# Optimization experiments

Hardware: AMD Instinct MI355X
Metric: run time of the kernel (lower is better)

## Reference

```python
import jax, jax.numpy as jnp
import numpy as np

N, E = 25000, 400000
D, H, L = 64, 4, 3
DH = D  # per-head out dim (concat=False averages heads)
NODE_IN, EDGE_IN = 16, 4


def setup_inputs() -> dict:
    key = jax.random.key(0)
    ks = jax.random.split(key, 24)
    s = 0.05
    inp = {
        "node_feat_in": jax.random.normal(ks[0], (N, NODE_IN), jnp.float32),
        "edge_index_in": jax.random.randint(ks[1], (2, E), 0, N, jnp.int32),
        "edge_attr_in": jax.random.normal(ks[2], (E, EDGE_IN), jnp.float32),
        # initial embeddings
        "W_node": jax.random.normal(ks[3], (NODE_IN, D), jnp.float32) * s,
        "b_node": jnp.zeros((D,), jnp.float32),
        "W_edge": jax.random.normal(ks[4], (EDGE_IN, D), jnp.float32) * s,
        "b_edge": jnp.zeros((D,), jnp.float32),
        # GATv2Conv params, stacked over layers
        "Wl": jax.random.normal(ks[5], (L, D, H * DH), jnp.float32) * s,
        "bl": jnp.zeros((L, H * DH), jnp.float32),
        "Wr": jax.random.normal(ks[6], (L, D, H * DH), jnp.float32) * s,
        "br": jnp.zeros((L, H * DH), jnp.float32),
        "We": jax.random.normal(ks[7], (L, D, H * DH), jnp.float32) * s,
        "att": jax.random.normal(ks[8], (L, H, DH), jnp.float32) * s,
        "conv_b": jnp.zeros((L, D), jnp.float32),
        # LayerNorm
        "ln_g": jnp.ones((L, D), jnp.float32),
        "ln_b": jnp.zeros((L, D), jnp.float32),
        # edge update MLP: Linear(3D->D), ReLU, Linear(D->D)
        "euW1": jax.random.normal(ks[9], (L, 3 * D, D), jnp.float32) * s,
        "eub1": jnp.zeros((L, D), jnp.float32),
        "euW2": jax.random.normal(ks[10], (L, D, D), jnp.float32) * s,
        "eub2": jnp.zeros((L, D), jnp.float32),
    }
    return inp


def _layernorm(x, g, b, eps=1e-5):
    mu = x.mean(-1, keepdims=True)
    var = ((x - mu) ** 2).mean(-1, keepdims=True)
    return (x - mu) * jax.lax.rsqrt(var + eps) * g + b


def _gatv2_conv(x, e, row, col, Wl, bl, Wr, br, We, att, cb):
    # PyG GATv2Conv(concat=False, edge_dim=D), eval mode (no dropout),
    # add_self_loops=True with fill_value='mean' on edge_attr.
    n = x.shape[0]
    xl = (x @ Wl + bl).reshape(n, H, DH)  # source transform
    xr = (x @ Wr + br).reshape(n, H, DH)  # target transform
    # self-loop edge attr = per-target mean of incoming edge attrs
    cnt = jax.ops.segment_sum(jnp.ones((e.shape[0],), x.dtype), col, num_segments=n)
    e_loop = jax.ops.segment_sum(e, col, num_segments=n) / jnp.maximum(cnt, 1.0)[:, None]
    ee = (jnp.concatenate([e, e_loop], 0) @ We).reshape(-1, H, DH)
    loop = jnp.arange(n, dtype=row.dtype)
    rowf = jnp.concatenate([row, loop])
    colf = jnp.concatenate([col, loop])
    msg = xl[rowf] + xr[colf] + ee                      # [E+N, H, DH]
    score = jnp.sum(jax.nn.leaky_relu(msg, 0.2) * att, -1)  # [E+N, H]
    # segment softmax over incoming edges of each target node
    m = jax.ops.segment_max(score, colf, num_segments=n)
    a = jnp.exp(score - m[colf])
    a = a / jax.ops.segment_sum(a, colf, num_segments=n)[colf]
    out = jax.ops.segment_sum(a[..., None] * xl[rowf], colf, num_segments=n)  # [N,H,DH]
    return out.mean(1) + cb  # concat=False -> head mean, plus bias


def reference(node_feat_in, edge_index_in, edge_attr_in, W_node, b_node, W_edge,
              b_edge, Wl, bl, Wr, br, We, att, conv_b, ln_g, ln_b, euW1, eub1,
              euW2, eub2):
    row, col = edge_index_in[0], edge_index_in[1]
    x = jax.nn.relu(node_feat_in @ W_node + b_node)
    e = jax.nn.relu(edge_attr_in @ W_edge + b_edge)
    for i in range(L):
        upd = _gatv2_conv(x, e, row, col, Wl[i], bl[i], Wr[i], br[i], We[i],
                          att[i], conv_b[i])
        x = jax.nn.relu(_layernorm(x + upd, ln_g[i], ln_b[i]))
        eu_in = jnp.concatenate([x[row], x[col], e], -1)  # [E, 3D]
        e_upd = jax.nn.relu(eu_in @ euW1[i] + eub1[i]) @ euW2[i] + eub2[i]
        e = jax.nn.relu(e + e_upd)
    return x, e
```

## Files before the change

kernel.cpp:

```cpp
#include <hip/hip_runtime.h>
#include <hip/hip_bf16.h>
#include <cstdint>
#include <cstddef>

constexpr int kN  = 25000;
constexpr int kE  = 400000;
constexpr int kEN = kE + kN;
constexpr int kD  = 64;
constexpr int kH  = 4;
constexpr int kHD = 256;

typedef __attribute__((ext_vector_type(8))) short short8;
typedef __attribute__((ext_vector_type(4))) float f32x4;

__device__ __forceinline__ float lrelu02(float x){ return x > 0.f ? x : 0.2f*x; }
__device__ __forceinline__ unsigned short f2bf(float f){
  __hip_bfloat16 h = __float2bfloat16(f);
  return *reinterpret_cast<unsigned short*>(&h);
}
__device__ __forceinline__ float bf2f(unsigned short u){
  return __uint_as_float(((unsigned)u) << 16);
}
__device__ __forceinline__ float bf_lo(unsigned u){ return __uint_as_float(u << 16); }
__device__ __forceinline__ float bf_hi(unsigned u){ return __uint_as_float(u & 0xffff0000u); }
__device__ __forceinline__ unsigned pack_bf2(float a, float b){
  return ((unsigned)f2bf(a)) | (((unsigned)f2bf(b)) << 16);
}

__global__ void k_deg(const int* __restrict__ col, int* __restrict__ deg){
  int i = blockIdx.x*256 + threadIdx.x;
  if (i < kE) atomicAdd(&deg[col[i]], 1);
}

__global__ void k_scan(const int* __restrict__ deg, int* __restrict__ col_start){
  __shared__ int lds[1024];
  __shared__ int carry_s;
  int t = threadIdx.x;
  if (t == 0) carry_s = 0;
  __syncthreads();
  for (int base = 0; base < kN; base += 1024){
    int v = (base + t < kN) ? deg[base + t] : 0;
    lds[t] = v; __syncthreads();
    for (int off = 1; off < 1024; off <<= 1){
      int add = (t >= off) ? lds[t - off] : 0;
      __syncthreads();
      lds[t] += add;
      __syncthreads();
    }
    int incl = lds[t];
    int carry = carry_s;
    if (base + t < kN) col_start[base + t] = carry + incl - v;
    __syncthreads();
    if (t == 0) carry_s = carry + lds[1023];
    __syncthreads();
  }
  if (t == 0) col_start[kN] = carry_s;
}

__global__ void k_fill(const int* __restrict__ col, const int* __restrict__ col_start,
                       int* __restrict__ fill, int* __restrict__ edge_ids){
  int i = blockIdx.x*256 + threadIdx.x;
  if (i < kE){
    int c = col[i];
    int p = atomicAdd(&fill[c], 1);
    edge_ids[col_start[c] + p] = i;
  }
}

__global__ void k_permrc(const int* __restrict__ edge_ids, const int* __restrict__ row,
                         const int* __restrict__ col, int* __restrict__ rowp,
                         int* __restrict__ colp){
  int p = blockIdx.x*256 + threadIdx.x;
  if (p < kE){
    int eid = edge_ids[p];
    rowp[p] = row[eid];
    colp[p] = col[eid];
  }
}

__global__ void k_prep(const float* __restrict__ We, unsigned short* __restrict__ WeT){
  int idx = blockIdx.x*256 + threadIdx.x;
  if (idx >= 3*256*64) return;
  int l = idx >> 14, j = (idx >> 6) & 255, k = idx & 63;
  WeT[idx] = f2bf(We[(size_t)l*16384 + k*256 + j]);
}

__global__ void k_prep2(const float* __restrict__ euW1, const float* __restrict__ euW2,
                        unsigned short* __restrict__ W1cT, unsigned short* __restrict__ W2T){
  int idx = blockIdx.x*256 + threadIdx.x;
  if (idx >= 3*64*64) return;
  int l = idx >> 12, rem = idx & 4095, d = rem >> 6, k = rem & 63;
  W1cT[idx] = f2bf(euW1[(size_t)l*192*64 + (size_t)(128+k)*64 + d]);
  W2T[idx]  = f2bf(euW2[(size_t)l*64*64  + (size_t)k*64 + d]);
}

__global__ void k_x0(const float* __restrict__ nf, const float* __restrict__ W,
                     const float* __restrict__ b, float* __restrict__ x){
  int i = blockIdx.x*256 + threadIdx.x;
  if (i >= kN*kD) return;
  int n = i >> 6, d = i & 63;
  float acc = b[d];
#pragma unroll
  for (int k = 0; k < 16; k++) acc += nf[n*16 + k] * W[k*64 + d];
  x[i] = fmaxf(acc, 0.f);
}

__global__ void k_e0p(const int* __restrict__ edge_ids,
                      const float* __restrict__ ea, const float* __restrict__ W,
                      const float* __restrict__ b,
                      unsigned short* __restrict__ ebf_perm){
  long long i = (long long)blockIdx.x*256 + threadIdx.x;
  if (i >= (long long)kE*kD) return;
  int p = (int)(i >> 6), d = (int)(i & 63);
  int eid = edge_ids[p];
  float acc = b[d];
#pragma unroll
  for (int k = 0; k < 4; k++) acc += ea[eid*4 + k] * W[k*64 + d];
  ebf_perm[i] = f2bf(fmaxf(acc, 0.f));
}

#define XLR_NPB 8
__global__ __launch_bounds__(256) void k_xlr(const float* __restrict__ x,
    const float* __restrict__ Wl, const float* __restrict__ bl,
    const float* __restrict__ Wr, const float* __restrict__ br,
    unsigned short* __restrict__ xl_bf, unsigned short* __restrict__ xr_bf){
  __shared__ float xs[XLR_NPB*64];
  int j = threadIdx.x;
  int n0 = blockIdx.x * XLR_NPB;
  for (int i = j; i < XLR_NPB*64; i += 256){
    int n = n0 + (i >> 6);
    xs[i] = (n < kN) ? x[(size_t)n*64 + (i & 63)] : 0.f;
  }
  __syncthreads();
  float accl[XLR_NPB], accr[XLR_NPB];
  float blv = bl[j], brv = br[j];
#pragma unroll
  for (int t = 0; t < XLR_NPB; t++){ accl[t] = blv; accr[t] = brv; }
  for (int k = 0; k < 64; k++){
    float wl = Wl[k*kHD + j], wr = Wr[k*kHD + j];
#pragma unroll
    for (int t = 0; t < XLR_NPB; t++){
      float xv = xs[t*64 + k];
      accl[t] += xv * wl; accr[t] += xv * wr;
    }
  }
#pragma unroll
  for (int t = 0; t < XLR_NPB; t++){
    int n = n0 + t;
    if (n < kN){
      xl_bf[(size_t)n*kHD + j] = f2bf(accl[t]);
      xr_bf[(size_t)n*kHD + j] = f2bf(accr[t]);
    }
  }
}

__global__ __launch_bounds__(256) void k_eloop(const unsigned short* __restrict__ ebf_perm,
    const int* __restrict__ col_start, unsigned short* __restrict__ eloop_bf){
  int wave = threadIdx.x >> 6, lane = threadIdx.x & 63;
  int n = blockIdx.x*4 + wave;
  if (n >= kN) return;
  int s0 = col_start[n], s1 = col_start[n+1];
  float acc = 0.f;
  for (int p = s0; p < s1; p++)
    acc += bf2f(ebf_perm[(size_t)p*64 + lane]);
  int dg = s1 - s0;
  eloop_bf[(size_t)n*64 + lane] = f2bf(acc / (float)(dg > 0 ? dg : 1));
}

struct STile {
  short8 b0, b1;
  uint2 xlu[4], xru[4];
};

__device__ __forceinline__ void s_load(int tile, STile& f, int e16, int kb, int h,
    const unsigned short* __restrict__ ebf_perm,
    const unsigned short* __restrict__ eloop_bf,
    const unsigned short* __restrict__ xl_bf,
    const unsigned short* __restrict__ xr_bf,
    const int* __restrict__ rowp, const int* __restrict__ colp)
{
  int p = tile*16 + e16;
  int pc = (p < kEN) ? p : 0;
  bool isE = pc < kE;
  const unsigned short* erow = isE ? (ebf_perm + (size_t)pc*64)
                                   : (eloop_bf + (size_t)(pc - kE)*64);
  f.b0 = *(const short8*)(erow + kb*8);
  f.b1 = *(const short8*)(erow + 32 + kb*8);
  int r = isE ? rowp[pc] : (pc - kE);
  int c = isE ? colp[pc] : (pc - kE);
  const unsigned short* xl_ = xl_bf + (size_t)r*kHD + h*64;
  const unsigned short* xr_ = xr_bf + (size_t)c*kHD + h*64;
#pragma unroll
  for (int mt = 0; mt < 4; mt++){
    f.xlu[mt] = *(const uint2*)(xl_ + mt*16 + kb*4);
    f.xru[mt] = *(const uint2*)(xr_ + mt*16 + kb*4);
  }
}

__device__ __forceinline__ void s_comp(int tile, const STile& f,
    const short8 A[4][2], const uint2 attp[4], int lane, int h,
    float* __restrict__ score)
{
  float sc = 0.f;
#pragma unroll
  for (int mt = 0; mt < 4; mt++){
    f32x4 acc = {0.f,0.f,0.f,0.f};
    acc = __builtin_amdgcn_mfma_f32_16x16x32_bf16(A[mt][0], f.b0, acc, 0, 0, 0);
    acc = __builtin_amdgcn_mfma_f32_16x16x32_bf16(A[mt][1], f.b1, acc, 0, 0, 0);
    sc += lrelu02(acc[0] + bf_lo(f.xlu[mt].x) + bf_lo(f.xru[mt].x)) * bf_lo(attp[mt].x);
    sc += lrelu02(acc[1] + bf_hi(f.xlu[mt].x) + bf_hi(f.xru[mt].x)) * bf_hi(attp[mt].x);
    sc += lrelu02(acc[2] + bf_lo(f.xlu[mt].y) + bf_lo(f.xru[mt].y)) * bf_lo(attp[mt].y);
    sc += lrelu02(acc[3] + bf_hi(f.xlu[mt].y) + bf_hi(f.xru[mt].y)) * bf_hi(attp[mt].y);
  }
  sc += __shfl_xor(sc, 16);
  sc += __shfl_xor(sc, 32);
  int wp = tile*16 + lane;
  if (lane < 16 && wp < kEN) score[(size_t)wp*kH + h] = sc;
}

__global__ __launch_bounds__(256) void k_score_mfma(
    const unsigned short* __restrict__ ebf_perm,
    const unsigned short* __restrict__ eloop_bf,
    const unsigned short* __restrict__ xl_bf,
    const unsigned short* __restrict__ xr_bf,
    const int* __restrict__ rowp, const int* __restrict__ colp,
    const unsigned short* __restrict__ WeT,
    const float* __restrict__ att,
    float* __restrict__ score)
{
  int lane = threadIdx.x & 63;
  int h    = threadIdx.x >> 6;
  int e16  = lane & 15;
  int kb   = lane >> 4;

  short8 A[4][2];
  uint2 attp[4];
#pragma unroll
  for (int mt = 0; mt < 4; mt++){
    const unsigned short* arow = WeT + (size_t)(h*64 + mt*16 + e16)*64 + kb*8;
    A[mt][0] = *(const short8*)(arow);
    A[mt][1] = *(const short8*)(arow + 32);
    f32x4 av = *(const f32x4*)(att + h*64 + mt*16 + kb*4);
    attp[mt].x = pack_bf2(av[0], av[1]);
    attp[mt].y = pack_bf2(av[2], av[3]);
  }

  constexpr int NT = (kEN + 15)/16;
  const int G = gridDim.x;
  STile fA, fB;
  int t0 = blockIdx.x;
  if (t0 < NT) s_load(t0, fA, e16, kb, h, ebf_perm, eloop_bf, xl_bf, xr_bf, rowp, colp);
  for (int tile = t0; tile < NT; tile += 2*G){
    int t1 = tile + G;
    if (t1 < NT) s_load(t1, fB, e16, kb, h, ebf_perm, eloop_bf, xl_bf, xr_bf, rowp, colp);
    s_comp(tile, fA, A, attp, lane, h, score);
    if (t1 < NT){
      int t2 = tile + 2*G;
      if (t2 < NT) s_load(t2, fA, e16, kb, h, ebf_perm, eloop_bf, xl_bf, xr_bf, rowp, colp);
      s_comp(t1, fB, A, attp, lane, h, score);
    }
  }
}

__global__ void k_segmax(const float* __restrict__ score,
    const int* __restrict__ col_start,
    float* __restrict__ aw, float* __restrict__ inv_s){
  int i = blockIdx.x*256 + threadIdx.x;
  if (i >= kN*kH) return;
  int n = i >> 2, h = i & 3;
  float selfsc = score[(size_t)(kE + n)*kH + h];
  float m = selfsc;
  int s0 = col_start[n], s1 = col_start[n+1];
  for (int p = s0; p < s1; p++)
    m = fmaxf(m, score[(size_t)p*kH + h]);
  float s = expf(selfsc - m);
  aw[(size_t)(kE + n)*kH + h] = s;
  for (int p = s0; p < s1; p++){
    float w = expf(score[(size_t)p*kH + h] - m);
    aw[(size_t)p*kH + h] = w;
    s += w;
  }
  inv_s[i] = 1.f / s;
}

__global__ __launch_bounds__(256) void k_agg_ln(
    const unsigned short* __restrict__ xl_bf, const float* __restrict__ aw,
    const float* __restrict__ inv_s,
    const int* __restrict__ rowp, const int* __restrict__ col_start,
    const float* __restrict__ conv_b, const float* __restrict__ ln_g,
    const float* __restrict__ ln_b, float* __restrict__ x){
  int n = blockIdx.x;
  int j = threadIdx.x, h = j >> 6, d = j & 63;
  float inv = inv_s[n*4 + h];
  float acc = aw[(size_t)(kE + n)*kH + h] * bf2f(xl_bf[(size_t)n*kHD + j]);
  int s0 = col_start[n], s1 = col_start[n+1];
  int p = s0;
  for (; p + 4 <= s1; p += 4){
    int r0 = rowp[p],   r1 = rowp[p+1], r2 = rowp[p+2], r3 = rowp[p+3];
    float a0 = aw[(size_t)p*kH + h],     a1 = aw[(size_t)(p+1)*kH + h];
    float a2 = aw[(size_t)(p+2)*kH + h], a3 = aw[(size_t)(p+3)*kH + h];
    float v0 = bf2f(xl_bf[(size_t)r0*kHD + j]);
    float v1 = bf2f(xl_bf[(size_t)r1*kHD + j]);
    float v2 = bf2f(xl_bf[(size_t)r2*kHD + j]);
    float v3 = bf2f(xl_bf[(size_t)r3*kHD + j]);
    acc += a0*v0; acc += a1*v1; acc += a2*v2; acc += a3*v3;
  }
  for (; p < s1; p++)
    acc += aw[(size_t)p*kH + h] * bf2f(xl_bf[(size_t)rowp[p]*kHD + j]);
  acc *= inv;

  __shared__ float lds[256];
  lds[j] = acc; __syncthreads();
  if (j < 64){
    float upd = (lds[d] + lds[64+d] + lds[128+d] + lds[192+d]) * 0.25f + conv_b[d];
    float y = x[(size_t)n*64 + d] + upd;
    float mu = y;
#pragma unroll
    for (int off = 32; off; off >>= 1) mu += __shfl_xor(mu, off);
    mu *= (1.f/64.f);
    float diff = y - mu;
    float var = diff * diff;
#pragma unroll
    for (int off = 32; off; off >>= 1) var += __shfl_xor(var, off);
    var *= (1.f/64.f);
    float out = diff * rsqrtf(var + 1e-5f) * ln_g[d] + ln_b[d];
    x[(size_t)n*64 + d] = fmaxf(out, 0.f);
  }
}

#define PQ_NPB 16
__global__ __launch_bounds__(256) void k_pq(const float* __restrict__ x,
    const float* __restrict__ W1, const float* __restrict__ b1,
    float* __restrict__ P, float* __restrict__ Q){
  __shared__ float xs[PQ_NPB*64];
  int tid = threadIdx.x;
  int j = tid & 63;
  int s = tid >> 6;
  int n0 = blockIdx.x * PQ_NPB;
  for (int i = tid; i < PQ_NPB*64; i += 256){
    int n = n0 + (i >> 6);
    xs[i] = (n < kN) ? x[(size_t)n*64 + (i & 63)] : 0.f;
  }
  __syncthreads();
  float accP[4], accQ[4];
  float b1v = b1[j];
#pragma unroll
  for (int t = 0; t < 4; t++){ accP[t] = b1v; accQ[t] = 0.f; }
  for (int k = 0; k < 64; k++){
    float wa = W1[k*64 + j];
    float wb = W1[(64 + k)*64 + j];
#pragma unroll
    for (int t = 0; t < 4; t++){
      float xv = xs[(s*4 + t)*64 + k];
      accP[t] += xv * wa; accQ[t] += xv * wb;
    }
  }
#pragma unroll
  for (int t = 0; t < 4; t++){
    int n = n0 + s*4 + t;
    if (n < kN){ P[(size_t)n*64 + j] = accP[t]; Q[(size_t)n*64 + j] = accQ[t]; }
  }
}

__global__ __launch_bounds__(256) void k_mlp_mfma(
    unsigned short* __restrict__ ebf_perm,
    float* __restrict__ eout_scatter,
    const int* __restrict__ edge_ids,
    const float* __restrict__ P, const float* __restrict__ Q,
    const unsigned short* __restrict__ W1cT,
    const unsigned short* __restrict__ W2T,
    const float* __restrict__ b2,
    const int* __restrict__ rowp, const int* __restrict__ colp)
{
  __shared__ unsigned short Hl[4][1024];
  int lane = threadIdx.x & 63, wv = threadIdx.x >> 6;
  int e16 = lane & 15, g = lane >> 4;
  int swz = (e16 & 7) << 4;
  char* Hw = (char*)Hl[wv];
  bool last = (eout_scatter != nullptr);

  short8 a1[4][2], a2[4][2];
#pragma unroll
  for (int mt = 0; mt < 4; mt++){
#pragma unroll
    for (int c = 0; c < 2; c++){
      a1[mt][c] = *(const short8*)(W1cT + (size_t)(mt*16 + e16)*64 + c*32 + g*8);
      a2[mt][c] = *(const short8*)(W2T  + (size_t)(mt*16 + e16)*64 + c*32 + g*8);
    }
  }
  f32x4 b2v[4];
#pragma unroll
  for (int mt = 0; mt < 4; mt++) b2v[mt] = *(const f32x4*)(b2 + mt*16 + g*4);

  int wid = (blockIdx.x*256 + threadIdx.x) >> 6;
  int nw  = (gridDim.x*256) >> 6;
  for (int tile = wid; tile < kE/16; tile += nw){
    int p = tile*16 + e16;
    int r = rowp[p], c = colp[p];
    const unsigned short* erow = ebf_perm + (size_t)p*64;
    short8 eb0 = *(const short8*)(erow + g*8);
    short8 eb1 = *(const short8*)(erow + 32 + g*8);
    const float* Pr = P + (size_t)r*64;
    const float* Qc = Q + (size_t)c*64;

#pragma unroll
    for (int mt = 0; mt < 4; mt++){
      f32x4 acc = {0.f,0.f,0.f,0.f};
      acc = __builtin_amdgcn_mfma_f32_16x16x32_bf16(a1[mt][0], eb0, acc, 0, 0, 0);
      acc = __builtin_amdgcn_mfma_f32_16x16x32_bf16(a1[mt][1], eb1, acc, 0, 0, 0);
      f32x4 pv = *(const f32x4*)(Pr + mt*16 + g*4);
      f32x4 qv = *(const f32x4*)(Qc + mt*16 + g*4);
      float h0 = fmaxf(acc[0] + pv[0] + qv[0], 0.f);
      float h1 = fmaxf(acc[1] + pv[1] + qv[1], 0.f);
      float h2 = fmaxf(acc[2] + pv[2] + qv[2], 0.f);
      float h3 = fmaxf(acc[3] + pv[3] + qv[3], 0.f);
      uint2 pk; pk.x = pack_bf2(h0, h1); pk.y = pack_bf2(h2, h3);
      *(uint2*)(Hw + (((e16 << 7) + (mt << 5) + (g << 3)) ^ swz)) = pk;
    }
    short8 hb0 = *(const short8*)(Hw + (((e16 << 7)      + (g << 4)) ^ swz));
    short8 hb1 = *(const short8*)(Hw + (((e16 << 7) + 64 + (g << 4)) ^ swz));

    int oe = last ? edge_ids[p] : 0;
#pragma unroll
    for (int mt = 0; mt < 4; mt++){
      f32x4 o = {0.f,0.f,0.f,0.f};
      o = __builtin_amdgcn_mfma_f32_16x16x32_bf16(a2[mt][0], hb0, o, 0, 0, 0);
      o = __builtin_amdgcn_mfma_f32_16x16x32_bf16(a2[mt][1], hb1, o, 0, 0, 0);
      size_t off = (size_t)p*64 + mt*16 + g*4;
      uint2 u = *(const uint2*)(ebf_perm + off);
      f32x4 eo;
      eo[0] = bf_lo(u.x); eo[1] = bf_hi(u.x); eo[2] = bf_lo(u.y); eo[3] = bf_hi(u.y);
      f32x4 ne;
      ne[0] = fmaxf(eo[0] + o[0] + b2v[mt][0], 0.f);
      ne[1] = fmaxf(eo[1] + o[1] + b2v[mt][1], 0.f);
      ne[2] = fmaxf(eo[2] + o[2] + b2v[mt][2], 0.f);
      ne[3] = fmaxf(eo[3] + o[3] + b2v[mt][3], 0.f);
      if (!last){
        uint2 po; po.x = pack_bf2(ne[0], ne[1]); po.y = pack_bf2(ne[2], ne[3]);
        *(uint2*)(ebf_perm + off) = po;
      } else {
        *(f32x4*)(eout_scatter + (size_t)oe*64 + mt*16 + g*4) = ne;
      }
    }
  }
}

extern "C" void kernel_launch(void* const* d_in, const int* in_sizes, int n_in,
                              void* d_out, int out_size, void* d_ws, size_t ws_size,
                              hipStream_t stream) {
  const float* node_feat = (const float*)d_in[0];
  const int*   edge_idx  = (const int*)d_in[1];
  const float* edge_attr = (const float*)d_in[2];
  const float* W_node = (const float*)d_in[3];
  const float* b_node = (const float*)d_in[4];
  const float* W_edge = (const float*)d_in[5];
  const float* b_edge = (const float*)d_in[6];
  const float* Wl   = (const float*)d_in[7];
  const float* bl   = (const float*)d_in[8];
  const float* Wr   = (const float*)d_in[9];
  const float* br   = (const float*)d_in[10];
  const float* We   = (const float*)d_in[11];
  const float* att  = (const float*)d_in[12];
  const float* cvb  = (const float*)d_in[13];
  const float* lng  = (const float*)d_in[14];
  const float* lnb  = (const float*)d_in[15];
  const float* euW1 = (const float*)d_in[16];
  const float* eub1 = (const float*)d_in[17];
  const float* euW2 = (const float*)d_in[18];
  const float* eub2 = (const float*)d_in[19];

  const int* row = edge_idx;
  const int* col = edge_idx + kE;

  float* x = (float*)d_out;
  float* e_out = (float*)d_out + (size_t)kN*kD;

  char* p = (char*)d_ws;
  auto carve = [&](size_t bytes)->void*{
    void* r = (void*)p;
    p += (bytes + 255) & ~(size_t)255;
    return r;
  };
  unsigned short* xl_bf    = (unsigned short*)carve((size_t)kN*kHD*2);
  unsigned short* xr_bf    = (unsigned short*)carve((size_t)kN*kHD*2);
  float* P      = (float*)carve((size_t)kN*kD*4);
  float* Q      = (float*)carve((size_t)kN*kD*4);
  unsigned short* ebf_perm = (unsigned short*)carve((size_t)kE*kD*2);
  unsigned short* eloop_bf = (unsigned short*)carve((size_t)kN*kD*2);
  unsigned short* WeT      = (unsigned short*)carve((size_t)3*kHD*kD*2);
  unsigned short* W1cT     = (unsigned short*)carve((size_t)3*kD*kD*2);
  unsigned short* W2T      = (unsigned short*)carve((size_t)3*kD*kD*2);
  float* score  = (float*)carve((size_t)kEN*kH*4);
  float* aw     = (float*)carve((size_t)kEN*kH*4);
  float* inv_s  = (float*)carve((size_t)kN*kH*4);
  int* deg      = (int*)carve((size_t)kN*4);
  int* col_start= (int*)carve((size_t)(kN+1)*4);
  int* fill     = (int*)carve((size_t)kN*4);
  int* edge_ids = (int*)carve((size_t)kE*4);
  int* rowp     = (int*)carve((size_t)kE*4);
  int* colp     = (int*)carve((size_t)kE*4);

  hipMemsetAsync(deg, 0, (size_t)kN*4, stream);
  hipMemsetAsync(fill, 0, (size_t)kN*4, stream);
  k_deg<<<(kE+255)/256, 256, 0, stream>>>(col, deg);
  k_scan<<<1, 1024, 0, stream>>>(deg, col_start);
  k_fill<<<(kE+255)/256, 256, 0, stream>>>(col, col_start, fill, edge_ids);
  k_permrc<<<(kE+255)/256, 256, 0, stream>>>(edge_ids, row, col, rowp, colp);

  k_prep<<<192, 256, 0, stream>>>(We, WeT);
  k_prep2<<<48, 256, 0, stream>>>(euW1, euW2, W1cT, W2T);
  k_x0<<<(kN*kD+255)/256, 256, 0, stream>>>(node_feat, W_node, b_node, x);
  k_e0p<<<(int)(((size_t)kE*kD+255)/256), 256, 0, stream>>>(edge_ids, edge_attr, W_edge,
                                                            b_edge, ebf_perm);

  for (int i = 0; i < 3; i++){
    const float* Wl_i  = Wl  + (size_t)i*kD*kHD;
    const float* bl_i  = bl  + (size_t)i*kHD;
    const float* Wr_i  = Wr  + (size_t)i*kD*kHD;
    const float* br_i  = br  + (size_t)i*kHD;
    const float* att_i = att + (size_t)i*kHD;
    const float* cvb_i = cvb + (size_t)i*kD;
    const float* lng_i = lng + (size_t)i*kD;
    const float* lnb_i = lnb + (size_t)i*kD;
    const float* W1_i  = euW1 + (size_t)i*192*64;
    const float* b1_i  = eub1 + (size_t)i*kD;
    const float* b2_i  = eub2 + (size_t)i*kD;
    const unsigned short* WeT_i  = WeT  + (size_t)i*kHD*kD;
    const unsigned short* W1cT_i = W1cT + (size_t)i*kD*kD;
    const unsigned short* W2T_i  = W2T  + (size_t)i*kD*kD;

    k_xlr<<<(kN + XLR_NPB - 1)/XLR_NPB, 256, 0, stream>>>(x, Wl_i, bl_i, Wr_i, br_i,
                                                          xl_bf, xr_bf);
    k_eloop<<<(kN + 3)/4, 256, 0, stream>>>(ebf_perm, col_start, eloop_bf);
    k_score_mfma<<<2048, 256, 0, stream>>>(ebf_perm, eloop_bf, xl_bf, xr_bf,
                                           rowp, colp, WeT_i, att_i, score);
    k_segmax<<<(kN*kH + 255)/256, 256, 0, stream>>>(score, col_start, aw, inv_s);
    k_agg_ln<<<kN, 256, 0, stream>>>(xl_bf, aw, inv_s, rowp, col_start,
                                     cvb_i, lng_i, lnb_i, x);
    k_pq<<<(kN + PQ_NPB - 1)/PQ_NPB, 256, 0, stream>>>(x, W1_i, b1_i, P, Q);
    k_mlp_mfma<<<2048, 256, 0, stream>>>(ebf_perm, (i < 2) ? nullptr : e_out,
                                         edge_ids, P, Q, W1cT_i, W2T_i, b2_i,
                                         rowp, colp);
  }
}
```

Measured before the change: 1.060 ms.

## Pack row/col indices, store P/Q as bf16, use contiguous XCD-aware tile chunks

Row and column indices are interleaved into an int2 array so score and MLP kernels issue one index load instead of two. P and Q from the edge-MLP projection are stored in bf16, halving their gather traffic in the MLP kernel at some precision cost. Both score and MLP kernels switch from grid-strided tiles to contiguous per-block tile ranges, with block IDs remapped so neighbouring chunks land on the same XCD for L2 locality. k_score_mfma also gets an occupancy hint in launch bounds.

Measured after the change: 1.089 ms. 1.03x slower.

```diff
diff --git a/kernel.cpp b/kernel.cpp
--- a/kernel.cpp
+++ b/kernel.cpp
@@ -69,12 +69,13 @@
 
 __global__ void k_permrc(const int* __restrict__ edge_ids, const int* __restrict__ row,
                          const int* __restrict__ col, int* __restrict__ rowp,
-                         int* __restrict__ colp){
+                         int2* __restrict__ rc2){
   int p = blockIdx.x*256 + threadIdx.x;
   if (p < kE){
     int eid = edge_ids[p];
-    rowp[p] = row[eid];
-    colp[p] = col[eid];
+    int r = row[eid], c = col[eid];
+    rowp[p] = r;
+    rc2[p] = make_int2(r, c);
   }
 }
 
@@ -177,19 +178,20 @@
     const unsigned short* __restrict__ eloop_bf,
     const unsigned short* __restrict__ xl_bf,
     const unsigned short* __restrict__ xr_bf,
-    const int* __restrict__ rowp, const int* __restrict__ colp)
+    const int2* __restrict__ rc2)
 {
   int p = tile*16 + e16;
   int pc = (p < kEN) ? p : 0;
   bool isE = pc < kE;
+  int2 rc;
+  if (isE) rc = rc2[pc];
+  else { rc.x = pc - kE; rc.y = pc - kE; }
   const unsigned short* erow = isE ? (ebf_perm + (size_t)pc*64)
                                    : (eloop_bf + (size_t)(pc - kE)*64);
   f.b0 = *(const short8*)(erow + kb*8);
   f.b1 = *(const short8*)(erow + 32 + kb*8);
-  int r = isE ? rowp[pc] : (pc - kE);
-  int c = isE ? colp[pc] : (pc - kE);
-  const unsigned short* xl_ = xl_bf + (size_t)r*kHD + h*64;
-  const unsigned short* xr_ = xr_bf + (size_t)c*kHD + h*64;
+  const unsigned short* xl_ = xl_bf + (size_t)rc.x*kHD + h*64;
+  const unsigned short* xr_ = xr_bf + (size_t)rc.y*kHD + h*64;
 #pragma unroll
   for (int mt = 0; mt < 4; mt++){
     f.xlu[mt] = *(const uint2*)(xl_ + mt*16 + kb*4);
@@ -218,12 +220,12 @@
   if (lane < 16 && wp < kEN) score[(size_t)wp*kH + h] = sc;
 }
 
-__global__ __launch_bounds__(256) void k_score_mfma(
+__global__ __launch_bounds__(256, 4) void k_score_mfma(
     const unsigned short* __restrict__ ebf_perm,
     const unsigned short* __restrict__ eloop_bf,
     const unsigned short* __restrict__ xl_bf,
     const unsigned short* __restrict__ xr_bf,
-    const int* __restrict__ rowp, const int* __restrict__ colp,
+    const int2* __restrict__ rc2,
     const unsigned short* __restrict__ WeT,
     const float* __restrict__ att,
     float* __restrict__ score)
@@ -246,19 +248,23 @@
   }
 
   constexpr int NT = (kEN + 15)/16;
-  const int G = gridDim.x;
-  STile fA, fB;
-  int t0 = blockIdx.x;
-  if (t0 < NT) s_load(t0, fA, e16, kb, h, ebf_perm, eloop_bf, xl_bf, xr_bf, rowp, colp);
-  for (int tile = t0; tile < NT; tile += 2*G){
-    int t1 = tile + G;
-    if (t1 < NT) s_load(t1, fB, e16, kb, h, ebf_perm, eloop_bf, xl_bf, xr_bf, rowp, colp);
-    s_comp(tile, fA, A, attp, lane, h, score);
-    if (t1 < NT){
-      int t2 = tile + 2*G;
-      if (t2 < NT) s_load(t2, fA, e16, kb, h, ebf_perm, eloop_bf, xl_bf, xr_bf, rowp, colp);
-      s_comp(t1, fB, A, attp, lane, h, score);
-    }
+  int nblk = gridDim.x;
+  int vb = (blockIdx.x & 7)*(nblk >> 3) + (blockIdx.x >> 3);
+  int cpb = (NT + nblk - 1)/nblk;
+  int t0 = vb*cpb;
+  int tend = min(t0 + cpb, NT);
+  int t = t0;
+  for (; t + 2 <= tend; t += 2){
+    STile fA, fB;
+    s_load(t,   fA, e16, kb, h, ebf_perm, eloop_bf, xl_bf, xr_bf, rc2);
+    s_load(t+1, fB, e16, kb, h, ebf_perm, eloop_bf, xl_bf, xr_bf, rc2);
+    s_comp(t,   fA, A, attp, lane, h, score);
+    s_comp(t+1, fB, A, attp, lane, h, score);
+  }
+  if (t < tend){
+    STile fA;
+    s_load(t, fA, e16, kb, h, ebf_perm, eloop_bf, xl_bf, xr_bf, rc2);
+    s_comp(t, fA, A, attp, lane, h, score);
   }
 }
 
@@ -331,7 +337,7 @@
 #define PQ_NPB 16
 __global__ __launch_bounds__(256) void k_pq(const float* __restrict__ x,
     const float* __restrict__ W1, const float* __restrict__ b1,
-    float* __restrict__ P, float* __restrict__ Q){
+    unsigned short* __restrict__ P_bf, unsigned short* __restrict__ Q_bf){
   __shared__ float xs[PQ_NPB*64];
   int tid = threadIdx.x;
   int j = tid & 63;
@@ -358,7 +364,10 @@
 #pragma unroll
   for (int t = 0; t < 4; t++){
     int n = n0 + s*4 + t;
-    if (n < kN){ P[(size_t)n*64 + j] = accP[t]; Q[(size_t)n*64 + j] = accQ[t]; }
+    if (n < kN){
+      P_bf[(size_t)n*64 + j] = f2bf(accP[t]);
+      Q_bf[(size_t)n*64 + j] = f2bf(accQ[t]);
+    }
   }
 }
 
@@ -366,11 +375,11 @@
     unsigned short* __restrict__ ebf_perm,
     float* __restrict__ eout_scatter,
     const int* __restrict__ edge_ids,
-    const float* __restrict__ P, const float* __restrict__ Q,
+    const unsigned short* __restrict__ P_bf, const unsigned short* __restrict__ Q_bf,
     const unsigned short* __restrict__ W1cT,
     const unsigned short* __restrict__ W2T,
     const float* __restrict__ b2,
-    const int* __restrict__ rowp, const int* __restrict__ colp)
+    const int2* __restrict__ rc2)
 {
   __shared__ unsigned short Hl[4][1024];
   int lane = threadIdx.x & 63, wv = threadIdx.x >> 6;
@@ -392,28 +401,32 @@
 #pragma unroll
   for (int mt = 0; mt < 4; mt++) b2v[mt] = *(const f32x4*)(b2 + mt*16 + g*4);
 
-  int wid = (blockIdx.x*256 + threadIdx.x) >> 6;
-  int nw  = (gridDim.x*256) >> 6;
-  for (int tile = wid; tile < kE/16; tile += nw){
+  constexpr int NT = kE/16;
+  int nblk = gridDim.x;
+  int vb = (blockIdx.x & 7)*(nblk >> 3) + (blockIdx.x >> 3);
+  int cpb = (NT + nblk - 1)/nblk;
+  int t0 = vb*cpb;
+  int tend = min(t0 + cpb, NT);
+  for (int tile = t0 + wv; tile < tend; tile += 4){
     int p = tile*16 + e16;
-    int r = rowp[p], c = colp[p];
+    int2 rc = rc2[p];
     const unsigned short* erow = ebf_perm + (size_t)p*64;
     short8 eb0 = *(const short8*)(erow + g*8);
     short8 eb1 = *(const short8*)(erow + 32 + g*8);
-    const float* Pr = P + (size_t)r*64;
-    const float* Qc = Q + (size_t)c*64;
+    const unsigned short* Pr = P_bf + (size_t)rc.x*64;
+    const unsigned short* Qc = Q_bf + (size_t)rc.y*64;
 
 #pragma unroll
     for (int mt = 0; mt < 4; mt++){
       f32x4 acc = {0.f,0.f,0.f,0.f};
       acc = __builtin_amdgcn_mfma_f32_16x16x32_bf16(a1[mt][0], eb0, acc, 0, 0, 0);
       acc = __builtin_amdgcn_mfma_f32_16x16x32_bf16(a1[mt][1], eb1, acc, 0, 0, 0);
-      f32x4 pv = *(const f32x4*)(Pr + mt*16 + g*4);
-      f32x4 qv = *(const f32x4*)(Qc + mt*16 + g*4);
-      float h0 = fmaxf(acc[0] + pv[0] + qv[0], 0.f);
-      float h1 = fmaxf(acc[1] + pv[1] + qv[1], 0.f);
-      float h2 = fmaxf(acc[2] + pv[2] + qv[2], 0.f);
-      float h3 = fmaxf(acc[3] + pv[3] + qv[3], 0.f);
+      uint2 pu = *(const uint2*)(Pr + mt*16 + g*4);
+      uint2 qu = *(const uint2*)(Qc + mt*16 + g*4);
+      float h0 = fmaxf(acc[0] + bf_lo(pu.x) + bf_lo(qu.x), 0.f);
+      float h1 = fmaxf(acc[1] + bf_hi(pu.x) + bf_hi(qu.x), 0.f);
+      float h2 = fmaxf(acc[2] + bf_lo(pu.y) + bf_lo(qu.y), 0.f);
+      float h3 = fmaxf(acc[3] + bf_hi(pu.y) + bf_hi(qu.y), 0.f);
       uint2 pk; pk.x = pack_bf2(h0, h1); pk.y = pack_bf2(h2, h3);
       *(uint2*)(Hw + (((e16 << 7) + (mt << 5) + (g << 3)) ^ swz)) = pk;
     }
@@ -483,8 +496,8 @@
   };
   unsigned short* xl_bf    = (unsigned short*)carve((size_t)kN*kHD*2);
   unsigned short* xr_bf    = (unsigned short*)carve((size_t)kN*kHD*2);
-  float* P      = (float*)carve((size_t)kN*kD*4);
-  float* Q      = (float*)carve((size_t)kN*kD*4);
+  unsigned short* P_bf     = (unsigned short*)carve((size_t)kN*kD*2);
+  unsigned short* Q_bf     = (unsigned short*)carve((size_t)kN*kD*2);
   unsigned short* ebf_perm = (unsigned short*)carve((size_t)kE*kD*2);
   unsigned short* eloop_bf = (unsigned short*)carve((size_t)kN*kD*2);
   unsigned short* WeT      = (unsigned short*)carve((size_t)3*kHD*kD*2);
@@ -498,14 +511,14 @@
   int* fill     = (int*)carve((size_t)kN*4);
   int* edge_ids = (int*)carve((size_t)kE*4);
   int* rowp     = (int*)carve((size_t)kE*4);
-  int* colp     = (int*)carve((size_t)kE*4);
+  int2* rc2     = (int2*)carve((size_t)kE*8);
 
   hipMemsetAsync(deg, 0, (size_t)kN*4, stream);
   hipMemsetAsync(fill, 0, (size_t)kN*4, stream);
   k_deg<<<(kE+255)/256, 256, 0, stream>>>(col, deg);
   k_scan<<<1, 1024, 0, stream>>>(deg, col_start);
   k_fill<<<(kE+255)/256, 256, 0, stream>>>(col, col_start, fill, edge_ids);
-  k_permrc<<<(kE+255)/256, 256, 0, stream>>>(edge_ids, row, col, rowp, colp);
+  k_permrc<<<(kE+255)/256, 256, 0, stream>>>(edge_ids, row, col, rowp, rc2);
 
   k_prep<<<192, 256, 0, stream>>>(We, WeT);
   k_prep2<<<48, 256, 0, stream>>>(euW1, euW2, W1cT, W2T);
@@ -533,13 +546,13 @@
                                                           xl_bf, xr_bf);
     k_eloop<<<(kN + 3)/4, 256, 0, stream>>>(ebf_perm, col_start, eloop_bf);
     k_score_mfma<<<2048, 256, 0, stream>>>(ebf_perm, eloop_bf, xl_bf, xr_bf,
-                                           rowp, colp, WeT_i, att_i, score);
+                                           rc2, WeT_i, att_i, score);
     k_segmax<<<(kN*kH + 255)/256, 256, 0, stream>>>(score, col_start, aw, inv_s);
     k_agg_ln<<<kN, 256, 0, stream>>>(xl_bf, aw, inv_s, rowp, col_start,
                                      cvb_i, lng_i, lnb_i, x);
-    k_pq<<<(kN + PQ_NPB - 1)/PQ_NPB, 256, 0, stream>>>(x, W1_i, b1_i, P, Q);
+    k_pq<<<(kN + PQ_NPB - 1)/PQ_NPB, 256, 0, stream>>>(x, W1_i, b1_i, P_bf, Q_bf);
     k_mlp_mfma<<<2048, 256, 0, stream>>>(ebf_perm, (i < 2) ? nullptr : e_out,
-                                         edge_ids, P, Q, W1cT_i, W2T_i, b2_i,
-                                         rowp, colp);
-  }
-}
+                                         edge_ids, P_bf, Q_bf, W1cT_i, W2T_i, b2_i,
+                                         rc2);
+  }
+}
```
